# Optimization experiments

Measured on AMD Instinct MI355X. Metric: run time of the kernel, lower is better.

The kernel has to match this reference:

```python
import jax, jax.numpy as jnp
import numpy as np
from itertools import combinations

# Module config: I=16, J=8 -> n_qubits = I + I + J = 40, k = 2
N_QUBITS = 40
K = 2
GATES = [(i, i + 1) for i in range(N_QUBITS - 1)]  # 39 RBS gates (ladder)
BATCH = 64


def _build_rbs_matrices():
    """Replicates RBS_Unitaries: for each gate (a,b) over the Hamming-weight-K
    basis of N_QUBITS qubits, build (A, B, C) with U(theta) = cos(theta)*A + sin(theta)*B + C.
    A: identity on states where exactly one of (a,b) is occupied (cos part).
    B: antisymmetric coupling swapping occupation of a<->b (sin part).
    C: identity on states where a,b have equal occupation (untouched part).
    """
    basis = list(combinations(range(N_QUBITS), K))
    idx = {s: i for i, s in enumerate(basis)}
    D = len(basis)  # binom(40, 2) = 780
    G = len(GATES)
    A = np.zeros((G, D, D), np.float32)
    B = np.zeros((G, D, D), np.float32)
    C = np.zeros((G, D, D), np.float32)
    for g, (a, b) in enumerate(GATES):
        for s in basis:
            i = idx[s]
            in_a, in_b = (a in s), (b in s)
            if in_a != in_b:
                A[g, i, i] = 1.0
                if in_a:  # pair |..1_a..0_b..> with |..0_a..1_b..>
                    t = tuple(sorted((set(s) - {a}) | {b}))
                    j = idx[t]
                    B[g, j, i] = 1.0
                    B[g, i, j] = -1.0
            else:
                C[g, i, i] = 1.0
    return A, B, C


def setup_inputs() -> dict:
    key = jax.random.key(0)
    k1, k2 = jax.random.split(key)
    A, B, C = _build_rbs_matrices()
    D = A.shape[-1]
    input_state = jax.random.normal(k1, (BATCH, D, D), dtype=jnp.float32)
    angles = jax.random.uniform(k2, (len(GATES),), dtype=jnp.float32)  # torch.rand(()) per gate
    return {
        "input_state": input_state,
        "angles": angles,
        "A": jnp.asarray(A),
        "B": jnp.asarray(B),
        "C": jnp.asarray(C),
    }


def reference(input_state, angles, A, B, C):
    """Sequentially applies each RBS gate: rho <- U rho U^T (real matrices)."""
    rho0 = input_state.astype(jnp.float32)

    def step(rho, gate):
        Ag, Bg, Cg, th = gate
        U = jnp.cos(th) * Ag + jnp.sin(th) * Bg + Cg  # [D, D]
        rho = jnp.einsum('ij,bjk->bik', U, rho)        # U @ rho
        rho = jnp.einsum('bik,lk->bil', rho, U)        # (U rho) @ U^T
        return rho, None

    out, _ = jax.lax.scan(step, rho0, (A, B, C, angles))
    return out
```

## Files before the change

### kernel.cpp

```cpp
#include <hip/hip_runtime.h>

#define D   780
#define NG  39
#define NP  38
#define KT  16
#define PAD 17

__device__ __forceinline__ int pair_idx(int p, int q) {
  return (p * (79 - p)) / 2 + (q - p - 1);
}

__global__ __launch_bounds__(256) void rbs_col_kernel(
    const float* __restrict__ rho, const float* __restrict__ ang,
    float* __restrict__ out) {
  __shared__ float csc[NG], css[NG];
  __shared__ float vbuf[4][D];
  const int tid = threadIdx.x;
  if (tid < NG) {
    float s, c;
    sincosf(ang[tid], &s, &c);
    csc[tid] = c; css[tid] = s;
  }
  __syncthreads();

  const int wave = tid >> 6, lane = tid & 63;
  const size_t row = (size_t)blockIdx.x * 4 + wave;
  const float4* src = (const float4*)(rho + row * (size_t)D);
  float* v = vbuf[wave];
  float4* v4 = (float4*)v;

  for (int e = lane; e < D / 4; e += 64) v4[e] = src[e];
  __builtin_amdgcn_wave_barrier();

  for (int g = 0; g < NG; ++g) {
    if (lane < NP) {
      const int cc = (lane < g) ? lane : lane + 2;
      const int a0 = (g  < cc) ? g  : cc,  a1 = (g  < cc) ? cc : g;
      const int g1 = g + 1;
      const int b0 = (g1 < cc) ? g1 : cc,  b1 = (g1 < cc) ? cc : g1;
      const int i = pair_idx(a0, a1);
      const int j = pair_idx(b0, b1);
      const float c = csc[g], s = css[g];
      const float vi = v[i], vj = v[j];
      v[i] = c * vi - s * vj;
      v[j] = s * vi + c * vj;
    }
    __builtin_amdgcn_wave_barrier();
  }

  float4* dst = (float4*)(out + row * (size_t)D);
  for (int e = lane; e < D / 4; e += 64) dst[e] = v4[e];
}

__global__ __launch_bounds__(512) void rbs_row_kernel(
    float* __restrict__ data, const float* __restrict__ ang) {
  __shared__ float csc[NG], css[NG];
  __shared__ float vb[D * PAD];
  const int tid = threadIdx.x;
  if (tid < NG) {
    float s, c;
    sincosf(ang[tid], &s, &c);
    csc[tid] = c; css[tid] = s;
  }
  const int b  = blockIdx.y;
  const int k0 = blockIdx.x * KT;
  const int ncols = (k0 + KT <= D) ? KT : (D - k0);
  float* base = data + (size_t)b * D * D + k0;

  const int fc = (tid & 3) * 4;
  const int r0 = tid >> 2;
  if (fc < ncols) {
    for (int r = r0; r < D; r += 128) {
      float4 x = *(const float4*)(base + (size_t)r * D + fc);
      float* p = &vb[r * PAD + fc];
      p[0] = x.x; p[1] = x.y; p[2] = x.z; p[3] = x.w;
    }
  }
  __syncthreads();

  const int pbase = tid >> 4;
  const int col   = tid & 15;
  for (int g = 0; g < NG; ++g) {
    const float c = csc[g], s = css[g];
    #pragma unroll
    for (int chunk = 0; chunk < 2; ++chunk) {
      const int pp = pbase + chunk * 32;
      if (pp < NP && col < ncols) {
        const int cc = (pp < g) ? pp : pp + 2;
        const int a0 = (g  < cc) ? g  : cc,  a1 = (g  < cc) ? cc : g;
        const int g1 = g + 1;
        const int b0 = (g1 < cc) ? g1 : cc,  b1 = (g1 < cc) ? cc : g1;
        const int i = pair_idx(a0, a1) * PAD + col;
        const int j = pair_idx(b0, b1) * PAD + col;
        const float vi = vb[i], vj = vb[j];
        vb[i] = c * vi - s * vj;
        vb[j] = s * vi + c * vj;
      }
    }
    __syncthreads();
  }

  if (fc < ncols) {
    for (int r = r0; r < D; r += 128) {
      float* p = &vb[r * PAD + fc];
      *(float4*)(base + (size_t)r * D + fc) = make_float4(p[0], p[1], p[2], p[3]);
    }
  }
}

extern "C" void kernel_launch(void* const* d_in, const int* in_sizes, int n_in,
                              void* d_out, int out_size, void* d_ws, size_t ws_size,
                              hipStream_t stream) {
  const float* rho = (const float*)d_in[0];
  const float* ang = (const float*)d_in[1];
  float* out = (float*)d_out;
  const int batch = in_sizes[0] / (D * D);

  const int nrows = batch * D;
  rbs_col_kernel<<<dim3(nrows / 4), 256, 0, stream>>>(rho, ang, out);

  rbs_row_kernel<<<dim3((D + KT - 1) / KT, batch), 512, 0, stream>>>(out, ang);
}
```

Baseline: 520.0 us.

## Transpose row-kernel tile so each wave owns one column with wave-level barriers

The row kernel's shared tile is now stored column-major ([KT][D]) and launched with 1024 threads, so each of the 16 waves processes one column independently. The 39 block-wide __syncthreads per gate become wave barriers, removing cross-wave synchronisation during the gate sweep. The cost is strided transposed writes and reads of shared memory during load and store, which may cause bank conflicts. Only 38 of 64 lanes are active per wave in the gate loop.

```diff
diff --git a/kernel.cpp b/kernel.cpp
--- a/kernel.cpp
+++ b/kernel.cpp
@@ -4,7 +4,6 @@
 #define NG  39
 #define NP  38
 #define KT  16
-#define PAD 17
 
 __device__ __forceinline__ int pair_idx(int p, int q) {
   return (p * (79 - p)) / 2 + (q - p - 1);
@@ -52,10 +51,10 @@
   for (int e = lane; e < D / 4; e += 64) dst[e] = v4[e];
 }
 
-__global__ __launch_bounds__(512) void rbs_row_kernel(
+__global__ __launch_bounds__(1024) void rbs_row_kernel(
     float* __restrict__ data, const float* __restrict__ ang) {
   __shared__ float csc[NG], css[NG];
-  __shared__ float vb[D * PAD];
+  __shared__ float vb[KT][D];
   const int tid = threadIdx.x;
   if (tid < NG) {
     float s, c;
@@ -64,46 +63,46 @@
   }
   const int b  = blockIdx.y;
   const int k0 = blockIdx.x * KT;
-  const int ncols = (k0 + KT <= D) ? KT : (D - k0);
+  const int ncols = (D - k0 < KT) ? (D - k0) : KT;
   float* base = data + (size_t)b * D * D + k0;
 
   const int fc = (tid & 3) * 4;
   const int r0 = tid >> 2;
   if (fc < ncols) {
-    for (int r = r0; r < D; r += 128) {
+    for (int r = r0; r < D; r += 256) {
       float4 x = *(const float4*)(base + (size_t)r * D + fc);
-      float* p = &vb[r * PAD + fc];
-      p[0] = x.x; p[1] = x.y; p[2] = x.z; p[3] = x.w;
+      vb[fc + 0][r] = x.x; vb[fc + 1][r] = x.y;
+      vb[fc + 2][r] = x.z; vb[fc + 3][r] = x.w;
     }
   }
   __syncthreads();
 
-  const int pbase = tid >> 4;
-  const int col   = tid & 15;
-  for (int g = 0; g < NG; ++g) {
-    const float c = csc[g], s = css[g];
-    #pragma unroll
-    for (int chunk = 0; chunk < 2; ++chunk) {
-      const int pp = pbase + chunk * 32;
-      if (pp < NP && col < ncols) {
-        const int cc = (pp < g) ? pp : pp + 2;
+  const int w = tid >> 6, lane = tid & 63;
+  if (w < ncols) {
+    float* v = vb[w];
+    for (int g = 0; g < NG; ++g) {
+      if (lane < NP) {
+        const int cc = (lane < g) ? lane : lane + 2;
         const int a0 = (g  < cc) ? g  : cc,  a1 = (g  < cc) ? cc : g;
         const int g1 = g + 1;
         const int b0 = (g1 < cc) ? g1 : cc,  b1 = (g1 < cc) ? cc : g1;
-        const int i = pair_idx(a0, a1) * PAD + col;
-        const int j = pair_idx(b0, b1) * PAD + col;
-        const float vi = vb[i], vj = vb[j];
-        vb[i] = c * vi - s * vj;
-        vb[j] = s * vi + c * vj;
+        const int i = pair_idx(a0, a1);
+        const int j = pair_idx(b0, b1);
+        const float c = csc[g], s = css[g];
+        const float vi = v[i], vj = v[j];
+        v[i] = c * vi - s * vj;
+        v[j] = s * vi + c * vj;
       }
+      __builtin_amdgcn_wave_barrier();
     }
-    __syncthreads();
   }
+  __syncthreads();
 
   if (fc < ncols) {
-    for (int r = r0; r < D; r += 128) {
-      float* p = &vb[r * PAD + fc];
-      *(float4*)(base + (size_t)r * D + fc) = make_float4(p[0], p[1], p[2], p[3]);
+    for (int r = r0; r < D; r += 256) {
+      float4 x = make_float4(vb[fc + 0][r], vb[fc + 1][r],
+                             vb[fc + 2][r], vb[fc + 3][r]);
+      *(float4*)(base + (size_t)r * D + fc) = x;
     }
   }
 }
@@ -119,5 +118,5 @@
   const int nrows = batch * D;
   rbs_col_kernel<<<dim3(nrows / 4), 256, 0, stream>>>(rho, ang, out);
 
-  rbs_row_kernel<<<dim3((D + KT - 1) / KT, batch), 512, 0, stream>>>(out, ang);
+  rbs_row_kernel<<<dim3((D + KT - 1) / KT, batch), 1024, 0, stream>>>(out, ang);
 }
```

Result: no change. 517.7 us (-0.5%).
